# Kernel tuning notes

Measured on AMD Instinct MI355X. Metric: run time of the kernel, lower is better.

The kernel has to match this reference:

```python
import jax, jax.numpy as jnp
import numpy as np

B, S, D_MODEL, H, NLAYERS, NHEADS = 16, 512, 768, 640, 2, 10
D_ATT = 2 * H  # 1280
HEAD_DIM = D_ATT // NHEADS  # 128


def _lstm_dir(xp, Whh, lengths, reverse):
    # xp: [B,S,4H] precomputed input projection (+bias); packed-sequence semantics:
    # state frozen and output zeroed for t >= length. torch gate order: i,f,g,o.
    Bs, Ss, H4 = xp.shape
    Hh = H4 // 4
    xpT = jnp.swapaxes(xp, 0, 1)  # [S,B,4H]
    ts = jnp.arange(Ss)
    if reverse:
        xpT = xpT[::-1]
        ts = ts[::-1]

    def step(carry, inp):
        h, c = carry
        x_t, t = inp
        g = x_t + h @ Whh.T
        i, f, gg, o = jnp.split(g, 4, axis=-1)
        i = jax.nn.sigmoid(i)
        f = jax.nn.sigmoid(f)
        gg = jnp.tanh(gg)
        o = jax.nn.sigmoid(o)
        c2 = f * c + i * gg
        h2 = o * jnp.tanh(c2)
        valid = (t < lengths)[:, None]
        h = jnp.where(valid, h2, h)
        c = jnp.where(valid, c2, c)
        return (h, c), jnp.where(valid, h, jnp.zeros_like(h))

    init = (jnp.zeros((Bs, Hh), xp.dtype), jnp.zeros((Bs, Hh), xp.dtype))
    _, ys = jax.lax.scan(step, init, (xpT, ts))
    if reverse:
        ys = ys[::-1]
    return jnp.swapaxes(ys, 0, 1)  # [B,S,H]


def _bilstm_layer(x, Wih, Whh, b, lengths):
    # Wih: [2,4H,in], Whh: [2,4H,H], b: [2,4H] (b_ih+b_hh combined)
    outs = []
    for d, rev in ((0, False), (1, True)):
        xp = jnp.einsum('bsi,gi->bsg', x, Wih[d]) + b[d]
        outs.append(_lstm_dir(xp, Whh[d], lengths, rev))
    return jnp.concatenate(outs, axis=-1)  # [B,S,2H]


def _forward(c_a_embeds, c_mask, c_lengths, Wih0, Whh0, b0, Wih1, Whh1, b1,
             Wq, bq, Wk, bk, Wv, bv):
    h = _bilstm_layer(c_a_embeds, Wih0, Whh0, b0, c_lengths)
    h = _bilstm_layer(h, Wih1, Whh1, b1, c_lengths)
    Bb, Ss, Dd = h.shape
    q = (h @ Wq.T + bq).reshape(Bb, Ss, NHEADS, HEAD_DIM)
    k = (h @ Wk.T + bk).reshape(Bb, Ss, NHEADS, HEAD_DIM)
    v = (h @ Wv.T + bv).reshape(Bb, Ss, NHEADS, HEAD_DIM)
    scores = jnp.einsum('bqhd,bkhd->bhqk', q, k) / np.float32(np.sqrt(HEAD_DIM))
    scores = scores + c_mask  # additive HF-style mask [B,1,1,S]
    probs = jax.nn.softmax(scores, axis=-1)
    ctx = jnp.einsum('bhqk,bkhd->bqhd', probs, v).reshape(Bb, Ss, Dd)
    return h + ctx


def setup_inputs() -> dict:
    key = jax.random.key(0)
    ks = jax.random.split(key, 20)
    c_a_embeds = jax.random.normal(ks[0], (B, S, D_MODEL), dtype=jnp.float32)
    c_lengths = jax.random.randint(ks[1], (B,), S // 2, S + 1, dtype=jnp.int32)
    valid = jnp.arange(S)[None, :] < c_lengths[:, None]
    c_mask = jnp.where(valid, 0.0, -10000.0).astype(jnp.float32)[:, None, None, :]
    sc = 1.0 / np.sqrt(H)

    def u(k, shape):
        return jax.random.uniform(k, shape, jnp.float32, -sc, sc)

    Wih0 = u(ks[2], (2, 4 * H, D_MODEL))
    Whh0 = u(ks[3], (2, 4 * H, H))
    b0 = u(ks[4], (2, 4 * H))
    Wih1 = u(ks[5], (2, 4 * H, 2 * H))
    Whh1 = u(ks[6], (2, 4 * H, H))
    b1 = u(ks[7], (2, 4 * H))
    sa = 1.0 / np.sqrt(D_ATT)
    Wq = jax.random.uniform(ks[8], (D_ATT, D_ATT), jnp.float32, -sa, sa)
    bq = jnp.zeros((D_ATT,), jnp.float32)
    Wk = jax.random.uniform(ks[9], (D_ATT, D_ATT), jnp.float32, -sa, sa)
    bk = jnp.zeros((D_ATT,), jnp.float32)
    Wv = jax.random.uniform(ks[10], (D_ATT, D_ATT), jnp.float32, -sa, sa)
    bv = jnp.zeros((D_ATT,), jnp.float32)
    return dict(c_a_embeds=c_a_embeds, c_mask=c_mask, c_lengths=c_lengths,
                Wih0=Wih0, Whh0=Whh0, b0=b0, Wih1=Wih1, Whh1=Whh1, b1=b1,
                Wq=Wq, bq=bq, Wk=Wk, bk=bk, Wv=Wv, bv=bv)


def reference(c_a_embeds, c_mask, c_lengths, Wih0, Whh0, b0, Wih1, Whh1, b1,
              Wq, bq, Wk, bk, Wv, bv):
    return _forward(c_a_embeds, c_mask, c_lengths, Wih0, Whh0, b0,
                    Wih1, Whh1, b1, Wq, bq, Wk, bk, Wv, bv)
```

## Files before the change

### kernel.cpp

```cpp
#include <hip/hip_runtime.h>

typedef __attribute__((ext_vector_type(8))) short short8;
typedef __attribute__((ext_vector_type(4))) float f32x4;
typedef __attribute__((ext_vector_type(4))) unsigned int u32x4;

#define MFMA(a,b,c) __builtin_amdgcn_mfma_f32_16x16x32_bf16((a),(b),(c),0,0,0)

#define B_  16
#define S_  512
#define DM_ 768
#define H_  640
#define G4_ 2560
#define DA_ 1280
#define NH_ 10
#define HD_ 128

static __device__ __forceinline__ unsigned short f2bf(float v) {
  unsigned u = __builtin_bit_cast(unsigned, v);
  u = (u + 0x7fffu + ((u >> 16) & 1u)) >> 16;
  return (unsigned short)u;
}
static __device__ __forceinline__ float bf2f(unsigned short u) {
  return __builtin_bit_cast(float, (unsigned)u << 16);
}
static __device__ __forceinline__ float sigm(float x) { return 1.0f / (1.0f + __expf(-x)); }
static __device__ __forceinline__ float tanh_c(float x) {
  x = fminf(fmaxf(x, -15.0f), 15.0f);
  float e = __expf(2.0f * x);
  return (e - 1.0f) / (e + 1.0f);
}

static __device__ __forceinline__ u32x4 load_coh16(const void* p) {
  u32x4 r;
  asm volatile("global_load_dwordx4 %0, %1, off sc0 sc1"
               : "=v"(r) : "v"(p) : "memory");
  return r;
}
static __device__ __forceinline__ void store_coh_u16(void* p, unsigned v) {
  asm volatile("global_store_short %0, %1, off sc0 sc1"
               :: "v"(p), "v"(v) : "memory");
}
static __device__ __forceinline__ void store_coh_u32(void* p, unsigned v) {
  asm volatile("global_store_dword %0, %1, off sc0 sc1"
               :: "v"(p), "v"(v) : "memory");
}
static __device__ __forceinline__ unsigned load_coh_u32(const void* p) {
  unsigned r;
  asm volatile("global_load_dword %0, %1, off sc0 sc1"
               : "=v"(r) : "v"(p) : "memory");
  return r;
}
#define WAIT_VM0() asm volatile("s_waitcnt vmcnt(0)" ::: "memory")

__global__ __launch_bounds__(256)
void cast_f32_bf16(const float* __restrict__ src, unsigned short* __restrict__ dst, int n4) {
  int i = blockIdx.x * 256 + threadIdx.x;
  if (i >= n4) return;
  float4 v = reinterpret_cast<const float4*>(src)[i];
  ushort4 o;
  o.x = f2bf(v.x); o.y = f2bf(v.y); o.z = f2bf(v.z); o.w = f2bf(v.w);
  reinterpret_cast<ushort4*>(dst)[i] = o;
}

__device__ __forceinline__ void gload_lds16(void* lds, const void* g) {
  __builtin_amdgcn_global_load_lds(
      (const __attribute__((address_space(1))) unsigned int*)g,
      (__attribute__((address_space(3))) unsigned int*)lds, 16, 0, 0);
}

template<int OUT_MODE>
__global__ __launch_bounds__(256)
void gemm_abt(const unsigned short* __restrict__ A, const unsigned short* __restrict__ W,
              const float* __restrict__ bias, void* __restrict__ Cout,
              int M, int N, int K) {
  __shared__ unsigned short lA[128 * 32];
  __shared__ unsigned short lB[128 * 32];
  const int tid = threadIdx.x;
  const int lane = tid & 63, wid = tid >> 6;
  const int nbn = N >> 7;
  const int mi = blockIdx.x / nbn, ni = blockIdx.x % nbn;
  const int l15 = lane & 15, lq = lane >> 4;

  f32x4 acc[4][4] = {};

  for (int k0 = 0; k0 < K; k0 += 32) {
#pragma unroll
    for (int part = 0; part < 2; ++part) {
      int linear = part * 256 + tid;
      int r = linear >> 2, cc = linear & 3;
      const unsigned short* ga = A + (size_t)(mi * 128 + r) * K + k0 + cc * 8;
      const unsigned short* gb = W + (size_t)(ni * 128 + r) * K + k0 + cc * 8;
      gload_lds16(&lA[(part * 256 + wid * 64) * 8], ga);
      gload_lds16(&lB[(part * 256 + wid * 64) * 8], gb);
    }
    __syncthreads();
    const int wm = (wid >> 1) * 64, wn = (wid & 1) * 64;
    short8 af[4], bfr[4];
#pragma unroll
    for (int m = 0; m < 4; ++m)
      af[m] = *(const short8*)&lA[(wm + m * 16 + l15) * 32 + lq * 8];
#pragma unroll
    for (int n = 0; n < 4; ++n)
      bfr[n] = *(const short8*)&lB[(wn + n * 16 + l15) * 32 + lq * 8];
#pragma unroll
    for (int m = 0; m < 4; ++m)
#pragma unroll
      for (int n = 0; n < 4; ++n)
        acc[m][n] = MFMA(af[m], bfr[n], acc[m][n]);
    __syncthreads();
  }

  const int wm = (wid >> 1) * 64, wn = (wid & 1) * 64;
#pragma unroll
  for (int n = 0; n < 4; ++n) {
    int col = ni * 128 + wn + n * 16 + l15;
    float bv = bias[col];
#pragma unroll
    for (int m = 0; m < 4; ++m) {
#pragma unroll
      for (int r = 0; r < 4; ++r) {
        int row = mi * 128 + wm + m * 16 + lq * 4 + r;
        float v = acc[m][n][r] + bv;
        if (OUT_MODE == 1) {
          ((unsigned short*)Cout)[(size_t)row * N + col] = f2bf(v);
        } else if (OUT_MODE == 2) {
          int bb = row >> 9, s = row & 511, hh = col >> 7, d = col & 127;
          ((unsigned short*)Cout)[(((size_t)(bb * NH_ + hh) * HD_ + d) << 9) + s] = f2bf(v);
        } else {
          int gate = col / 640, unit = col % 640;
          int slice = unit / 20, uu = unit % 20;
          int bb = row >> 9, tt = row & 511;
          size_t idx = (((size_t)slice * S_ + tt) * B_ + bb) * 80 + gate * 20 + uu;
          if (OUT_MODE == 3) ((float*)Cout)[idx] = v;
          else               ((unsigned short*)Cout)[idx] = f2bf(v);
        }
      }
    }
  }
}

template<bool XPF32>
__global__ __launch_bounds__(320)
void bilstm_layer(const void* __restrict__ xp_,
                  const unsigned short* __restrict__ whh_g,
                  const int* __restrict__ lengths,
                  unsigned short* __restrict__ h_ex,
                  int* __restrict__ flags, int flag_base,
                  unsigned short* __restrict__ out_bf)
{
  __shared__ unsigned short whh[80 * 648];
  __shared__ unsigned short hbuf[16 * 648];
  __shared__ float pre[16 * 80];
  __shared__ float xpbuf[16 * 80];
  __shared__ int len_s[16];

  const int tid = threadIdx.x;
  const int lane = tid & 63, wid = tid >> 6;
  const int wg = blockIdx.x;
  const int dir = wg >> 5, slice = wg & 31;
  const int J0 = slice * 20;
  const int l15 = lane & 15, lq = lane >> 4;

  for (int c = tid; c < 80 * 160; c += 320) {
    int r = c / 160, c4 = c % 160;
    int grow = (r / 20) * H_ + J0 + (r % 20);
    *(ushort4*)&whh[r * 648 + c4 * 4] =
        *(const ushort4*)&whh_g[((size_t)dir * G4_ + grow) * H_ + c4 * 4];
  }
  if (tid < 16) len_s[tid] = lengths[tid];
  __syncthreads();

  const int gb = tid / 20, gu = tid % 20;
  float c_st = 0.f, h_st = 0.f;

  const char* xps;
  if (XPF32)
    xps = (const char*)xp_ + ((size_t)dir * 32 + slice) * S_ * B_ * 80 * 4;
  else
    xps = (const char*)xp_ + ((size_t)dir * 32 + slice) * S_ * B_ * 80 * 2;

  float4  xv_f;
  ushort4 xv_h;
  {
    int t0 = dir ? (S_ - 1) : 0;
    if (XPF32) xv_f = *(const float4*)(xps + ((size_t)t0 * 1280 + tid * 4) * 4);
    else       xv_h = *(const ushort4*)(xps + ((size_t)t0 * 1280 + tid * 4) * 2);
  }

  for (int s = 0; s < S_; ++s) {
    const int t = dir ? (S_ - 1 - s) : s;
    float4  xn_f;
    ushort4 xn_h;
    {
      int tn = dir ? (S_ - 2 - s) : (s + 1);
      tn = tn < 0 ? 0 : (tn > S_ - 1 ? S_ - 1 : tn);
      if (XPF32) xn_f = *(const float4*)(xps + ((size_t)tn * 1280 + tid * 4) * 4);
      else       xn_h = *(const ushort4*)(xps + ((size_t)tn * 1280 + tid * 4) * 2);
    }

    {
      const unsigned short* src = h_ex + (size_t)(dir * 2 + (s & 1)) * B_ * H_;
      u32x4 hv[4];
      int bs[4], os[4];
#pragma unroll
      for (int j = 0; j < 4; ++j) {
        int c = tid + j * 320;
        bs[j] = c / 80; os[j] = c % 80;
        hv[j] = load_coh16(src + (size_t)bs[j] * 640 + os[j] * 8);
      }
      WAIT_VM0();
      __builtin_amdgcn_sched_barrier(0);
#pragma unroll
      for (int j = 0; j < 4; ++j)
        *(u32x4*)&hbuf[bs[j] * 648 + os[j] * 8] = hv[j];
    }
    if (XPF32) {
      *(float4*)&xpbuf[tid * 4] = xv_f;
    } else {
      *(ushort4*)&((unsigned short*)xpbuf)[tid * 4] = xv_h;
    }
    __syncthreads();

    f32x4 acc0 = {0.f, 0.f, 0.f, 0.f}, acc1 = {0.f, 0.f, 0.f, 0.f};
#pragma unroll
    for (int kk = 0; kk < 20; kk += 2) {
      short8 a0 = *(const short8*)&hbuf[l15 * 648 + kk * 32 + lq * 8];
      short8 b0v = *(const short8*)&whh[(wid * 16 + l15) * 648 + kk * 32 + lq * 8];
      acc0 = MFMA(a0, b0v, acc0);
      short8 a1 = *(const short8*)&hbuf[l15 * 648 + (kk + 1) * 32 + lq * 8];
      short8 b1v = *(const short8*)&whh[(wid * 16 + l15) * 648 + (kk + 1) * 32 + lq * 8];
      acc1 = MFMA(a1, b1v, acc1);
    }
#pragma unroll
    for (int r = 0; r < 4; ++r)
      pre[(lq * 4 + r) * 80 + wid * 16 + l15] = acc0[r] + acc1[r];
    __syncthreads();

    {
      float xi, xf, xg, xo;
      if (XPF32) {
        xi = xpbuf[gb * 80 + gu];
        xf = xpbuf[gb * 80 + 20 + gu];
        xg = xpbuf[gb * 80 + 40 + gu];
        xo = xpbuf[gb * 80 + 60 + gu];
      } else {
        const unsigned short* xb = (const unsigned short*)xpbuf;
        xi = bf2f(xb[gb * 80 + gu]);
        xf = bf2f(xb[gb * 80 + 20 + gu]);
        xg = bf2f(xb[gb * 80 + 40 + gu]);
        xo = bf2f(xb[gb * 80 + 60 + gu]);
      }
      float gi = pre[gb * 80 + gu]      + xi;
      float gf = pre[gb * 80 + 20 + gu] + xf;
      float gg = pre[gb * 80 + 40 + gu] + xg;
      float go = pre[gb * 80 + 60 + gu] + xo;
      float i_ = sigm(gi), f_ = sigm(gf);
      float g_ = tanh_c(gg), o_ = sigm(go);
      float c2 = f_ * c_st + i_ * g_;
      float h2 = o_ * tanh_c(c2);
      bool valid = t < len_s[gb];
      c_st = valid ? c2 : c_st;
      h_st = valid ? h2 : h_st;
      unsigned hb = f2bf(h_st);
      store_coh_u16(h_ex + (size_t)(dir * 2 + ((s + 1) & 1)) * B_ * H_
                         + (size_t)gb * H_ + J0 + gu, hb);
      float yv = valid ? h_st : 0.f;
      out_bf[((size_t)(gb * S_ + t)) * DA_ + dir * H_ + J0 + gu] = f2bf(yv);
    }

    WAIT_VM0();
    __syncthreads();
    const int target = flag_base + s + 1;
    if (tid == 0)
      store_coh_u32(flags + (size_t)wg * 32, (unsigned)target);
    if (wid == 0) {
      const int* fp = flags + (size_t)(dir * 32 + (lane & 31)) * 32;
      for (;;) {
        unsigned v = load_coh_u32(fp);
        WAIT_VM0();
        if (__all((int)v >= target)) break;
      }
    }
    __syncthreads();
    xv_f = xn_f; xv_h = xn_h;
  }
}

__global__ __launch_bounds__(256)
void attn_fused(const unsigned short* __restrict__ q, const unsigned short* __restrict__ k,
                const unsigned short* __restrict__ vT, const float* __restrict__ mask,
                const unsigned short* __restrict__ h1, float* __restrict__ out)
{
  __shared__ unsigned short p_lds[64 * 512];
  const int tid = threadIdx.x, lane = tid & 63, wid = tid >> 6;
  const int bx = blockIdx.x;
  const int b = bx / 80, rem = bx % 80, h = rem / 8, qt = rem % 8;
  const int l15 = lane & 15, lq = lane >> 4;
  const int qrow0 = qt * 64 + wid * 16;

  short8 qf[4];
  {
    const unsigned short* qb = q + ((size_t)(b * S_ + qrow0 + l15)) * DA_ + h * HD_ + lq * 8;
#pragma unroll
    for (int ks = 0; ks < 4; ++ks) qf[ks] = *(const short8*)(qb + ks * 32);
  }
  f32x4 sc[32];
#pragma unroll
  for (int nt = 0; nt < 32; ++nt) {
    f32x4 a = {0.f, 0.f, 0.f, 0.f};
    const unsigned short* kb = k + ((size_t)(b * S_ + nt * 16 + l15)) * DA_ + h * HD_ + lq * 8;
#pragma unroll
    for (int ks = 0; ks < 4; ++ks) {
      short8 bf = *(const short8*)(kb + ks * 32);
      a = MFMA(qf[ks], bf, a);
    }
    sc[nt] = a;
  }
  const float scl = 0.08838834764831845f;
  float mx[4] = {-1e30f, -1e30f, -1e30f, -1e30f};
#pragma unroll
  for (int nt = 0; nt < 32; ++nt) {
    float mv = mask[b * S_ + nt * 16 + l15];
#pragma unroll
    for (int r = 0; r < 4; ++r) {
      float v = sc[nt][r] * scl + mv;
      sc[nt][r] = v;
      mx[r] = fmaxf(mx[r], v);
    }
  }
#pragma unroll
  for (int r = 0; r < 4; ++r) {
    mx[r] = fmaxf(mx[r], __shfl_xor(mx[r], 1));
    mx[r] = fmaxf(mx[r], __shfl_xor(mx[r], 2));
    mx[r] = fmaxf(mx[r], __shfl_xor(mx[r], 4));
    mx[r] = fmaxf(mx[r], __shfl_xor(mx[r], 8));
  }
  float sm[4] = {0.f, 0.f, 0.f, 0.f};
#pragma unroll
  for (int nt = 0; nt < 32; ++nt)
#pragma unroll
    for (int r = 0; r < 4; ++r) {
      float p = __expf(sc[nt][r] - mx[r]);
      sc[nt][r] = p; sm[r] += p;
    }
#pragma unroll
  for (int r = 0; r < 4; ++r) {
    sm[r] += __shfl_xor(sm[r], 1);
    sm[r] += __shfl_xor(sm[r], 2);
    sm[r] += __shfl_xor(sm[r], 4);
    sm[r] += __shfl_xor(sm[r], 8);
    sm[r] = 1.0f / sm[r];
  }
#pragma unroll
  for (int nt = 0; nt < 32; ++nt)
#pragma unroll
    for (int r = 0; r < 4; ++r) {
      int row = wid * 16 + lq * 4 + r;
      int byte = row * 1024 + (nt * 16 + l15) * 2;
      byte ^= (row & 7) << 4;
      *(unsigned short*)((char*)p_lds + byte) = f2bf(sc[nt][r] * sm[r]);
    }
  __syncthreads();

  f32x4 oa[8] = {};
#pragma unroll
  for (int kk = 0; kk < 16; ++kk) {
    int row = wid * 16 + l15;
    int byte = row * 1024 + (kk * 32 + lq * 8) * 2;
    byte ^= (row & 7) << 4;
    short8 pa = *(const short8*)((char*)p_lds + byte);
    const unsigned short* vb = vT + ((size_t)(b * NH_ + h) * HD_ + l15) * S_ + kk * 32 + lq * 8;
#pragma unroll
    for (int n = 0; n < 8; ++n) {
      short8 bv = *(const short8*)(vb + n * 16 * S_);
      oa[n] = MFMA(pa, bv, oa[n]);
    }
  }
#pragma unroll
  for (int n = 0; n < 8; ++n)
#pragma unroll
    for (int r = 0; r < 4; ++r) {
      int row = qrow0 + lq * 4 + r;
      int col = h * HD_ + n * 16 + l15;
      size_t idx = ((size_t)(b * S_ + row)) * DA_ + col;
      out[idx] = bf2f(h1[idx]) + oa[n][r];
    }
}

extern "C" void kernel_launch(void* const* d_in, const int* in_sizes, int n_in,
                              void* d_out, int out_size, void* d_ws, size_t ws_size,
                              hipStream_t stream) {
  const float* x    = (const float*)d_in[0];
  const float* mask = (const float*)d_in[1];
  const int*   lens = (const int*)d_in[2];
  const float* Wih0 = (const float*)d_in[3];
  const float* Whh0 = (const float*)d_in[4];
  const float* b0   = (const float*)d_in[5];
  const float* Wih1 = (const float*)d_in[6];
  const float* Whh1 = (const float*)d_in[7];
  const float* b1   = (const float*)d_in[8];
  const float* Wq   = (const float*)d_in[9];
  const float* bq   = (const float*)d_in[10];
  const float* Wk   = (const float*)d_in[11];
  const float* bk   = (const float*)d_in[12];
  const float* Wv   = (const float*)d_in[13];
  const float* bv   = (const float*)d_in[14];

  const size_t SZ_wb_ih1 = (size_t)2 * G4_ * DA_ * 2;
  const size_t SZ_wb_hh  = (size_t)2 * G4_ * H_ * 2;
  const size_t SZ_wb_qkv = (size_t)DA_ * DA_ * 2;
  const size_t SZ_tok_bf = (size_t)B_ * S_ * DA_ * 2;
  const size_t SZ_h_ex   = (size_t)2 * 2 * B_ * H_ * 2;
  const size_t SZ_flags  = (size_t)64 * 32 * 4;
  const size_t SZ_xbf    = (size_t)B_ * S_ * DM_ * 2;
  const size_t SZ_wb_ih0 = (size_t)2 * G4_ * DM_ * 2;
  const size_t SZ_regA   = SZ_xbf + SZ_wb_ih0 + SZ_wb_hh;
  const size_t SZ_xp_f32 = (size_t)2 * B_ * S_ * G4_ * 4;
  const size_t SZ_xp_bf  = SZ_xp_f32 / 2;

  const size_t persist = SZ_wb_ih1 + SZ_wb_hh + 3 * SZ_wb_qkv + 2 * SZ_tok_bf
                       + SZ_h_ex + SZ_flags;
  const size_t need_A = persist + SZ_regA + SZ_xp_f32;
  const bool xpf32 = (ws_size >= need_A + 4096);

  char* ws = (char*)d_ws;
  size_t off = 0;
  auto alloc = [&](size_t bytes) { char* p = ws + off; off += bytes; return p; };

  unsigned short* wb_ih1 = (unsigned short*)alloc(SZ_wb_ih1);
  unsigned short* wb_hh1 = (unsigned short*)alloc(SZ_wb_hh);
  unsigned short* wb_q   = (unsigned short*)alloc(SZ_wb_qkv);
  unsigned short* wb_k   = (unsigned short*)alloc(SZ_wb_qkv);
  unsigned short* wb_v   = (unsigned short*)alloc(SZ_wb_qkv);
  unsigned short* h0bf   = (unsigned short*)alloc(SZ_tok_bf);
  unsigned short* h1bf   = (unsigned short*)alloc(SZ_tok_bf);
  unsigned short* h_ex   = (unsigned short*)alloc(SZ_h_ex);
  int*            flags  = (int*)alloc(SZ_flags);

  char* regA = alloc(SZ_regA);
  unsigned short* xbf    = (unsigned short*)regA;
  unsigned short* wb_ih0 = (unsigned short*)(regA + SZ_xbf);
  unsigned short* wb_hh0 = (unsigned short*)(regA + SZ_xbf + SZ_wb_ih0);
  unsigned short* qbf    = (unsigned short*)regA;

  char* regB = alloc(xpf32 ? SZ_xp_f32 : SZ_xp_bf);
  void*           xp     = (void*)regB;
  unsigned short* kbf    = (unsigned short*)regB;
  unsigned short* vtbf   = (unsigned short*)(regB + SZ_tok_bf);

  hipMemsetAsync(h_ex, 0, SZ_h_ex + SZ_flags, stream);

  auto cast = [&](const float* s, unsigned short* d, size_t n) {
    int n4 = (int)(n / 4);
    cast_f32_bf16<<<(n4 + 255) / 256, 256, 0, stream>>>(s, d, n4);
  };
  cast(Wih0, wb_ih0, (size_t)2 * G4_ * DM_);
  cast(Whh0, wb_hh0, (size_t)2 * G4_ * H_);
  cast(Wih1, wb_ih1, (size_t)2 * G4_ * DA_);
  cast(Whh1, wb_hh1, (size_t)2 * G4_ * H_);
  cast(Wq, wb_q, (size_t)DA_ * DA_);
  cast(Wk, wb_k, (size_t)DA_ * DA_);
  cast(Wv, wb_v, (size_t)DA_ * DA_);
  cast(x, xbf, (size_t)B_ * S_ * DM_);

  const int M = B_ * S_;
  const size_t xp_dir_elems = (size_t)32 * S_ * B_ * 80;

  if (xpf32) {
    gemm_abt<3><<<(M / 128) * (G4_ / 128), 256, 0, stream>>>(
        xbf, wb_ih0, b0, xp, M, G4_, DM_);
    gemm_abt<3><<<(M / 128) * (G4_ / 128), 256, 0, stream>>>(
        xbf, wb_ih0 + (size_t)G4_ * DM_, b0 + G4_,
        (float*)xp + xp_dir_elems, M, G4_, DM_);
    bilstm_layer<true><<<64, 320, 0, stream>>>(xp, wb_hh0, lens, h_ex, flags, 0, h0bf);
  } else {
    gemm_abt<4><<<(M / 128) * (G4_ / 128), 256, 0, stream>>>(
        xbf, wb_ih0, b0, xp, M, G4_, DM_);
    gemm_abt<4><<<(M / 128) * (G4_ / 128), 256, 0, stream>>>(
        xbf, wb_ih0 + (size_t)G4_ * DM_, b0 + G4_,
        (unsigned short*)xp + xp_dir_elems, M, G4_, DM_);
    bilstm_layer<false><<<64, 320, 0, stream>>>(xp, wb_hh0, lens, h_ex, flags, 0, h0bf);
  }

  if (xpf32) {
    gemm_abt<3><<<(M / 128) * (G4_ / 128), 256, 0, stream>>>(
        h0bf, wb_ih1, b1, xp, M, G4_, DA_);
    gemm_abt<3><<<(M / 128) * (G4_ / 128), 256, 0, stream>>>(
        h0bf, wb_ih1 + (size_t)G4_ * DA_, b1 + G4_,
        (float*)xp + xp_dir_elems, M, G4_, DA_);
  } else {
    gemm_abt<4><<<(M / 128) * (G4_ / 128), 256, 0, stream>>>(
        h0bf, wb_ih1, b1, xp, M, G4_, DA_);
    gemm_abt<4><<<(M / 128) * (G4_ / 128), 256, 0, stream>>>(
        h0bf, wb_ih1 + (size_t)G4_ * DA_, b1 + G4_,
        (unsigned short*)xp + xp_dir_elems, M, G4_, DA_);
  }
  hipMemsetAsync(h_ex, 0, SZ_h_ex, stream);
  if (xpf32)
    bilstm_layer<true><<<64, 320, 0, stream>>>(xp, wb_hh1, lens, h_ex, flags, S_, h1bf);
  else
    bilstm_layer<false><<<64, 320, 0, stream>>>(xp, wb_hh1, lens, h_ex, flags, S_, h1bf);

  gemm_abt<1><<<(M / 128) * (DA_ / 128), 256, 0, stream>>>(
      h1bf, wb_q, bq, qbf, M, DA_, DA_);
  gemm_abt<1><<<(M / 128) * (DA_ / 128), 256, 0, stream>>>(
      h1bf, wb_k, bk, kbf, M, DA_, DA_);
  gemm_abt<2><<<(M / 128) * (DA_ / 128), 256, 0, stream>>>(
      h1bf, wb_v, bv, vtbf, M, DA_, DA_);
  attn_fused<<<B_ * NH_ * 8, 256, 0, stream>>>(qbf, kbf, vtbf, mask, h1bf,
                                               (float*)d_out);
}
```

Before: 4.132 ms.

## Restructure LSTM step exchange: staged wide stores, single-wave publish, deferred output writes

The recurrent kernel now stages each step's hidden slice in LDS. One wave publishes it to the global exchange buffer with 64-bit coherent stores and then sets the progress flag. Another wave polls the flags in parallel, which removes the per-thread 16-bit coherent stores and the full vmcnt wait by all threads before signaling. The output write and the next-step input prefetch move after the handoff, and the closing barrier waits only on LDS, so global stores overlap the spin-wait. The exchange buffer is 20480 bytes per image, which equals the old B×H bf16 size, so the layout is unchanged; the memset is moved earlier. This relies on careful memory ordering between the publishing wave and the flag.

```diff
diff --git a/kernel.cpp b/kernel.cpp
--- a/kernel.cpp
+++ b/kernel.cpp
@@ -14,6 +14,7 @@
 #define DA_ 1280
 #define NH_ 10
 #define HD_ 128
+#define U_   20
 
 static __device__ __forceinline__ unsigned short f2bf(float v) {
   unsigned u = __builtin_bit_cast(unsigned, v);
@@ -36,21 +37,27 @@
                : "=v"(r) : "v"(p) : "memory");
   return r;
 }
-static __device__ __forceinline__ void store_coh_u16(void* p, unsigned v) {
-  asm volatile("global_store_short %0, %1, off sc0 sc1"
+static __device__ __forceinline__ void store_coh64(void* p, unsigned long long v) {
+  asm volatile("global_store_dwordx2 %0, %1, off sc0 sc1"
                :: "v"(p), "v"(v) : "memory");
 }
 static __device__ __forceinline__ void store_coh_u32(void* p, unsigned v) {
   asm volatile("global_store_dword %0, %1, off sc0 sc1"
                :: "v"(p), "v"(v) : "memory");
 }
-static __device__ __forceinline__ unsigned load_coh_u32(const void* p) {
+static __device__ __forceinline__ unsigned poll_u32(const void* p) {
   unsigned r;
-  asm volatile("global_load_dword %0, %1, off sc0 sc1"
+  asm volatile("global_load_dword %0, %1, off sc0 sc1\n\ts_waitcnt vmcnt(0)"
                : "=v"(r) : "v"(p) : "memory");
   return r;
 }
 #define WAIT_VM0() asm volatile("s_waitcnt vmcnt(0)" ::: "memory")
+
+static __device__ __forceinline__ void bar_lgkm() {
+  __builtin_amdgcn_sched_barrier(0);
+  asm volatile("s_waitcnt lgkmcnt(0)\n\ts_barrier" ::: "memory");
+  __builtin_amdgcn_sched_barrier(0);
+}
 
 __global__ __launch_bounds__(256)
 void cast_f32_bf16(const float* __restrict__ src, unsigned short* __restrict__ dst, int n4) {
@@ -144,21 +151,22 @@
 void bilstm_layer(const void* __restrict__ xp_,
                   const unsigned short* __restrict__ whh_g,
                   const int* __restrict__ lengths,
-                  unsigned short* __restrict__ h_ex,
-                  int* __restrict__ flags, int flag_base,
+                  char* __restrict__ h_ex,
+                  int* __restrict__ flags, int fb,
                   unsigned short* __restrict__ out_bf)
 {
   __shared__ unsigned short whh[80 * 648];
   __shared__ unsigned short hbuf[16 * 648];
   __shared__ float pre[16 * 80];
   __shared__ float xpbuf[16 * 80];
+  __shared__ unsigned short staged[16 * 20];
   __shared__ int len_s[16];
 
   const int tid = threadIdx.x;
-  const int lane = tid & 63, wid = tid >> 6;
+  const int lane = tid & 63, wv = tid >> 6;
   const int wg = blockIdx.x;
   const int dir = wg >> 5, slice = wg & 31;
-  const int J0 = slice * 20;
+  const int J0 = slice * U_;
   const int l15 = lane & 15, lq = lane >> 4;
 
   for (int c = tid; c < 80 * 160; c += 320) {
@@ -173,14 +181,10 @@
   const int gb = tid / 20, gu = tid % 20;
   float c_st = 0.f, h_st = 0.f;
 
-  const char* xps;
-  if (XPF32)
-    xps = (const char*)xp_ + ((size_t)dir * 32 + slice) * S_ * B_ * 80 * 4;
-  else
-    xps = (const char*)xp_ + ((size_t)dir * 32 + slice) * S_ * B_ * 80 * 2;
-
-  float4  xv_f;
-  ushort4 xv_h;
+  const char* xps = (const char*)xp_ +
+      ((size_t)dir * 32 + slice) * S_ * 1280 * (XPF32 ? 4 : 2);
+
+  float4  xv_f; ushort4 xv_h;
   {
     int t0 = dir ? (S_ - 1) : 0;
     if (XPF32) xv_f = *(const float4*)(xps + ((size_t)t0 * 1280 + tid * 4) * 4);
@@ -189,24 +193,15 @@
 
   for (int s = 0; s < S_; ++s) {
     const int t = dir ? (S_ - 1 - s) : s;
-    float4  xn_f;
-    ushort4 xn_h;
+
     {
-      int tn = dir ? (S_ - 2 - s) : (s + 1);
-      tn = tn < 0 ? 0 : (tn > S_ - 1 ? S_ - 1 : tn);
-      if (XPF32) xn_f = *(const float4*)(xps + ((size_t)tn * 1280 + tid * 4) * 4);
-      else       xn_h = *(const ushort4*)(xps + ((size_t)tn * 1280 + tid * 4) * 2);
-    }
-
-    {
-      const unsigned short* src = h_ex + (size_t)(dir * 2 + (s & 1)) * B_ * H_;
-      u32x4 hv[4];
-      int bs[4], os[4];
+      const char* src = h_ex + (size_t)((dir * 2 + (s & 1)) * 20480);
+      u32x4 hv[4]; int bs[4], os[4];
 #pragma unroll
       for (int j = 0; j < 4; ++j) {
         int c = tid + j * 320;
         bs[j] = c / 80; os[j] = c % 80;
-        hv[j] = load_coh16(src + (size_t)bs[j] * 640 + os[j] * 8);
+        hv[j] = load_coh16(src + (size_t)bs[j] * 1280 + os[j] * 16);
       }
       WAIT_VM0();
       __builtin_amdgcn_sched_barrier(0);
@@ -214,28 +209,26 @@
       for (int j = 0; j < 4; ++j)
         *(u32x4*)&hbuf[bs[j] * 648 + os[j] * 8] = hv[j];
     }
-    if (XPF32) {
-      *(float4*)&xpbuf[tid * 4] = xv_f;
-    } else {
-      *(ushort4*)&((unsigned short*)xpbuf)[tid * 4] = xv_h;
-    }
+    if (XPF32) *(float4*)&xpbuf[tid * 4] = xv_f;
+    else       *(ushort4*)&((unsigned short*)xpbuf)[tid * 4] = xv_h;
     __syncthreads();
 
     f32x4 acc0 = {0.f, 0.f, 0.f, 0.f}, acc1 = {0.f, 0.f, 0.f, 0.f};
 #pragma unroll
     for (int kk = 0; kk < 20; kk += 2) {
       short8 a0 = *(const short8*)&hbuf[l15 * 648 + kk * 32 + lq * 8];
-      short8 b0v = *(const short8*)&whh[(wid * 16 + l15) * 648 + kk * 32 + lq * 8];
+      short8 b0v = *(const short8*)&whh[(wv * 16 + l15) * 648 + kk * 32 + lq * 8];
       acc0 = MFMA(a0, b0v, acc0);
       short8 a1 = *(const short8*)&hbuf[l15 * 648 + (kk + 1) * 32 + lq * 8];
-      short8 b1v = *(const short8*)&whh[(wid * 16 + l15) * 648 + (kk + 1) * 32 + lq * 8];
+      short8 b1v = *(const short8*)&whh[(wv * 16 + l15) * 648 + (kk + 1) * 32 + lq * 8];
       acc1 = MFMA(a1, b1v, acc1);
     }
 #pragma unroll
     for (int r = 0; r < 4; ++r)
-      pre[(lq * 4 + r) * 80 + wid * 16 + l15] = acc0[r] + acc1[r];
+      pre[(lq * 4 + r) * 80 + wv * 16 + l15] = acc0[r] + acc1[r];
     __syncthreads();
 
+    float yv;
     {
       float xi, xf, xg, xo;
       if (XPF32) {
@@ -261,28 +254,46 @@
       bool valid = t < len_s[gb];
       c_st = valid ? c2 : c_st;
       h_st = valid ? h2 : h_st;
-      unsigned hb = f2bf(h_st);
-      store_coh_u16(h_ex + (size_t)(dir * 2 + ((s + 1) & 1)) * B_ * H_
-                         + (size_t)gb * H_ + J0 + gu, hb);
-      float yv = valid ? h_st : 0.f;
-      out_bf[((size_t)(gb * S_ + t)) * DA_ + dir * H_ + J0 + gu] = f2bf(yv);
-    }
-
-    WAIT_VM0();
+      staged[gb * 20 + gu] = f2bf(h_st);
+      yv = valid ? h_st : 0.f;
+    }
     __syncthreads();
-    const int target = flag_base + s + 1;
-    if (tid == 0)
-      store_coh_u32(flags + (size_t)wg * 32, (unsigned)target);
-    if (wid == 0) {
-      const int* fp = flags + (size_t)(dir * 32 + (lane & 31)) * 32;
-      for (;;) {
-        unsigned v = load_coh_u32(fp);
+
+    if (s + 1 < S_) {
+      if (wv == 4) {
+        char* img = h_ex + (size_t)((dir * 2 + ((s + 1) & 1)) * 20480);
+        {
+          int b = lane / 5, q = lane % 5;
+          unsigned long long d = *(const unsigned long long*)&staged[b * 20 + q * 4];
+          store_coh64(img + (size_t)b * 1280 + slice * 40 + q * 8, d);
+        }
+        if (lane < 16) {
+          int k2 = 64 + lane, b = k2 / 5, q = k2 % 5;
+          unsigned long long d = *(const unsigned long long*)&staged[b * 20 + q * 4];
+          store_coh64(img + (size_t)b * 1280 + slice * 40 + q * 8, d);
+        }
         WAIT_VM0();
-        if (__all((int)v >= target)) break;
+        if (lane == 0)
+          store_coh_u32(flags + (size_t)(dir * 32 + slice) * 32,
+                        (unsigned)(fb + s + 1));
+      } else if (wv == 0) {
+        const int tgt = fb + s + 1;
+        const int* fp = flags + (size_t)(dir * 32 + (lane & 31)) * 32;
+        for (;;) {
+          unsigned v = poll_u32(fp);
+          if (__all((int)v >= tgt)) break;
+        }
       }
     }
-    __syncthreads();
-    xv_f = xn_f; xv_h = xn_h;
+
+    out_bf[((size_t)(gb * S_ + t)) * DA_ + dir * H_ + J0 + gu] = f2bf(yv);
+    {
+      int tn = dir ? (S_ - 2 - s) : (s + 1);
+      tn = tn < 0 ? 0 : (tn > S_ - 1 ? S_ - 1 : tn);
+      if (XPF32) xv_f = *(const float4*)(xps + ((size_t)tn * 1280 + tid * 4) * 4);
+      else       xv_h = *(const ushort4*)(xps + ((size_t)tn * 1280 + tid * 4) * 2);
+    }
+    bar_lgkm();
   }
 }
 
@@ -410,7 +421,7 @@
   const size_t SZ_wb_hh  = (size_t)2 * G4_ * H_ * 2;
   const size_t SZ_wb_qkv = (size_t)DA_ * DA_ * 2;
   const size_t SZ_tok_bf = (size_t)B_ * S_ * DA_ * 2;
-  const size_t SZ_h_ex   = (size_t)2 * 2 * B_ * H_ * 2;
+  const size_t SZ_h_ex   = (size_t)2 * 2 * 20480;
   const size_t SZ_flags  = (size_t)64 * 32 * 4;
   const size_t SZ_xbf    = (size_t)B_ * S_ * DM_ * 2;
   const size_t SZ_wb_ih0 = (size_t)2 * G4_ * DM_ * 2;
@@ -434,7 +445,7 @@
   unsigned short* wb_v   = (unsigned short*)alloc(SZ_wb_qkv);
   unsigned short* h0bf   = (unsigned short*)alloc(SZ_tok_bf);
   unsigned short* h1bf   = (unsigned short*)alloc(SZ_tok_bf);
-  unsigned short* h_ex   = (unsigned short*)alloc(SZ_h_ex);
+  char*           h_ex   = alloc(SZ_h_ex);
   int*            flags  = (int*)alloc(SZ_flags);
 
   char* regA = alloc(SZ_regA);
@@ -464,7 +475,7 @@
   cast(x, xbf, (size_t)B_ * S_ * DM_);
 
   const int M = B_ * S_;
-  const size_t xp_dir_elems = (size_t)32 * S_ * B_ * 80;
+  const size_t xp_dir_elems = (size_t)32 * S_ * 1280;
 
   if (xpf32) {
     gemm_abt<3><<<(M / 128) * (G4_ / 128), 256, 0, stream>>>(
@@ -482,24 +493,23 @@
     bilstm_layer<false><<<64, 320, 0, stream>>>(xp, wb_hh0, lens, h_ex, flags, 0, h0bf);
   }
 
+  hipMemsetAsync(h_ex, 0, SZ_h_ex, stream);
+
   if (xpf32) {
     gemm_abt<3><<<(M / 128) * (G4_ / 128), 256, 0, stream>>>(
         h0bf, wb_ih1, b1, xp, M, G4_, DA_);
     gemm_abt<3><<<(M / 128) * (G4_ / 128), 256, 0, stream>>>(
         h0bf, wb_ih1 + (size_t)G4_ * DA_, b1 + G4_,
         (float*)xp + xp_dir_elems, M, G4_, DA_);
+    bilstm_layer<true><<<64, 320, 0, stream>>>(xp, wb_hh1, lens, h_ex, flags, S_, h1bf);
   } else {
     gemm_abt<4><<<(M / 128) * (G4_ / 128), 256, 0, stream>>>(
         h0bf, wb_ih1, b1, xp, M, G4_, DA_);
     gemm_abt<4><<<(M / 128) * (G4_ / 128), 256, 0, stream>>>(
         h0bf, wb_ih1 + (size_t)G4_ * DA_, b1 + G4_,
         (unsigned short*)xp + xp_dir_elems, M, G4_, DA_);
-  }
-  hipMemsetAsync(h_ex, 0, SZ_h_ex, stream);
-  if (xpf32)
-    bilstm_layer<true><<<64, 320, 0, stream>>>(xp, wb_hh1, lens, h_ex, flags, S_, h1bf);
-  else
     bilstm_layer<false><<<64, 320, 0, stream>>>(xp, wb_hh1, lens, h_ex, flags, S_, h1bf);
+  }
 
   gemm_abt<1><<<(M / 128) * (DA_ / 128), 256, 0, stream>>>(
       h1bf, wb_q, bq, qbf, M, DA_, DA_);
```

Result: no change. 4.213 ms (+2.0%).
